# Kernel tuning notes

Measured on AMD Instinct MI355X. Metric: run time of the kernel, lower is better.

## Reference

```python
import jax, jax.numpy as jnp
import numpy as np

N = 50000
E = 800000
IN_DIM, HID, HEADS, OUT_DIM = 32, 64, 4, 128
HC = HID * HEADS  # 256
LN_EPS = 1e-5
NEG_SLOPE = 0.2


def setup_inputs() -> dict:
    key = jax.random.key(0)
    ks = jax.random.split(key, 16)
    s = 0.05
    inp = {
        "x": jax.random.normal(ks[0], (N, IN_DIM), dtype=jnp.float32),
        "edge_index": jax.random.randint(ks[1], (2, E), 0, N, dtype=jnp.int32),
        # input projection
        "W_in": jax.random.normal(ks[2], (IN_DIM, HID), dtype=jnp.float32) * s,
        "b_in": jnp.zeros((HID,), dtype=jnp.float32),
        # GAT layer 0: in=HID, out=HID per head, HEADS heads
        "lin0_w": jax.random.normal(ks[3], (HID, HC), dtype=jnp.float32) * s,
        "att0_src": jax.random.normal(ks[4], (HEADS, HID), dtype=jnp.float32) * s,
        "att0_dst": jax.random.normal(ks[5], (HEADS, HID), dtype=jnp.float32) * s,
        "bias0": jnp.zeros((HC,), dtype=jnp.float32),
        # GAT layer 1: in=HC, out=HID per head
        "lin1_w": jax.random.normal(ks[6], (HC, HC), dtype=jnp.float32) * s,
        "att1_src": jax.random.normal(ks[7], (HEADS, HID), dtype=jnp.float32) * s,
        "att1_dst": jax.random.normal(ks[8], (HEADS, HID), dtype=jnp.float32) * s,
        "bias1": jnp.zeros((HC,), dtype=jnp.float32),
        # output projection + layernorm
        "W_out": jax.random.normal(ks[9], (HC, OUT_DIM), dtype=jnp.float32) * s,
        "b_out": jnp.zeros((OUT_DIM,), dtype=jnp.float32),
        "ln_gamma": jnp.ones((OUT_DIM,), dtype=jnp.float32),
        "ln_beta": jnp.zeros((OUT_DIM,), dtype=jnp.float32),
    }
    return inp


def _gat_conv(x, src, dst, lin_w, att_src, att_dst, bias):
    # x: [N, F_in]; src/dst: [E'] (self-loops included)
    h = (x @ lin_w).reshape(N, HEADS, HID)           # [N, H, C]
    a_src = jnp.einsum("nhc,hc->nh", h, att_src)      # [N, H]
    a_dst = jnp.einsum("nhc,hc->nh", h, att_dst)      # [N, H]
    e = a_src[src] + a_dst[dst]                        # [E', H]
    e = jnp.where(e > 0, e, NEG_SLOPE * e)             # leaky_relu(0.2)
    # segment softmax over incoming edges per destination
    m = jax.ops.segment_max(e, dst, num_segments=N)    # [N, H]
    p = jnp.exp(e - m[dst])
    denom = jax.ops.segment_sum(p, dst, num_segments=N)
    alpha = p / (denom[dst] + 1e-16)                   # [E', H]
    msg = h[src] * alpha[:, :, None]                   # [E', H, C]
    out = jax.ops.segment_sum(msg, dst, num_segments=N)  # [N, H, C]
    return out.reshape(N, HC) + bias


def reference(x, edge_index, W_in, b_in, lin0_w, att0_src, att0_dst, bias0,
              lin1_w, att1_src, att1_dst, bias1, W_out, b_out, ln_gamma, ln_beta):
    # add self-loops (PyG GATConv default)
    loops = jnp.arange(N, dtype=edge_index.dtype)
    src = jnp.concatenate([edge_index[0], loops])
    dst = jnp.concatenate([edge_index[1], loops])

    h = jax.nn.elu(x @ W_in + b_in)
    h = jax.nn.elu(_gat_conv(h, src, dst, lin0_w, att0_src, att0_dst, bias0))
    h = jax.nn.elu(_gat_conv(h, src, dst, lin1_w, att1_src, att1_dst, bias1))
    h = h @ W_out + b_out
    mu = jnp.mean(h, axis=-1, keepdims=True)
    var = jnp.mean((h - mu) ** 2, axis=-1, keepdims=True)
    return (h - mu) * jax.lax.rsqrt(var + LN_EPS) * ln_gamma + ln_beta
```

## Files before the change

### kernel.cpp

```cpp
#include <hip/hip_runtime.h>
#include <cstdint>

#define N_NODES 50000
#define N_EDGES 800000
#define EP (N_EDGES + N_NODES)
#define IN_DIM 32
#define HID 64
#define HEADS 4
#define HC 256
#define OUT_DIM 128
#define NEG_SLOPE 0.2f
#define LN_EPS 1e-5f
#define SCAN_B 1024
#define NB ((N_NODES + SCAN_B - 1) / SCAN_B)

typedef __attribute__((ext_vector_type(8))) short bf16x8;
typedef __attribute__((ext_vector_type(16))) float f32x16;

__device__ __forceinline__ unsigned bf16rne(float f) {
    unsigned u = __float_as_uint(f);
    return (u + 0x7fffu + ((u >> 16) & 1u)) >> 16;
}
__device__ __forceinline__ unsigned pack_bf2(float a, float b) {
    return bf16rne(a) | (bf16rne(b) << 16);
}
__device__ __forceinline__ float bf_lo(unsigned w) { return __uint_as_float(w << 16); }
__device__ __forceinline__ float bf_hi(unsigned w) { return __uint_as_float(w & 0xffff0000u); }

__global__ void k_in_proj(const float* __restrict__ x, const float* __restrict__ W,
                          const float* __restrict__ b, unsigned short* __restrict__ out) {
    int g = blockIdx.x * blockDim.x + threadIdx.x;
    int n = g >> 6, j = g & 63;
    const float* xr = x + n * IN_DIM;
    float acc = b[j];
#pragma unroll
    for (int k = 0; k < IN_DIM; ++k) acc += xr[k] * W[k * HID + j];
    acc = acc > 0.f ? acc : (__expf(acc) - 1.f);
    out[g] = (unsigned short)bf16rne(acc);
}

__global__ void k_wpack(const float* __restrict__ w0, const float* __restrict__ w1,
                        const float* __restrict__ w2, unsigned short* __restrict__ p0,
                        unsigned short* __restrict__ p1, unsigned short* __restrict__ p2) {
    int g = blockIdx.x * blockDim.x + threadIdx.x;
    if (g < HID * HC) {
        int k = g >> 8, n = g & 255;
        p0[(((k >> 3) * HC) + n) * 8 + (k & 7)] = (unsigned short)bf16rne(w0[g]);
    } else if (g < HID * HC + HC * HC) {
        int t = g - HID * HC;
        int k = t >> 8, n = t & 255;
        p1[(((k >> 3) * HC) + n) * 8 + (k & 7)] = (unsigned short)bf16rne(w1[t]);
    } else if (g < HID * HC + HC * HC + HC * OUT_DIM) {
        int t = g - HID * HC - HC * HC;
        int k = t >> 7, n = t & 127;
        p2[(((k >> 3) * OUT_DIM) + n) * 8 + (k & 7)] = (unsigned short)bf16rne(w2[t]);
    }
}

template <int K>
__global__ __launch_bounds__(256) void k_gemm_lin(
        const unsigned short* __restrict__ A, const unsigned short* __restrict__ Bp,
        unsigned short* __restrict__ hh) {
    const int lane = threadIdx.x & 63;
    const int quad = lane >> 5, c = lane & 31;
    const int wave = threadIdx.x >> 6;
    const int m0 = blockIdx.x * 64 + (wave >> 1) * 32;
    const int cb = (wave & 1) * 128;
    f32x16 acc[4];
#pragma unroll
    for (int nt = 0; nt < 4; ++nt)
#pragma unroll
        for (int i = 0; i < 16; ++i) acc[nt][i] = 0.f;
    int mrow = m0 + c; if (mrow >= N_NODES) mrow = N_NODES - 1;
    const size_t abase = (size_t)mrow * K + quad * 8;
    for (int k0 = 0; k0 < K; k0 += 16) {
        bf16x8 af = *(const bf16x8*)(A + abase + k0);
        const unsigned short* bk = Bp + ((size_t)(k0 >> 3) + quad) * (HC * 8);
#pragma unroll
        for (int nt = 0; nt < 4; ++nt) {
            bf16x8 bf = *(const bf16x8*)(bk + (cb + nt * 32 + c) * 8);
            acc[nt] = __builtin_amdgcn_mfma_f32_32x32x16_bf16(af, bf, acc[nt], 0, 0, 0);
        }
    }
#pragma unroll
    for (int reg = 0; reg < 16; ++reg) {
        int row = (reg & 3) + 8 * (reg >> 2) + 4 * quad;
        int m = m0 + row;
        if (m < N_NODES) {
            size_t base = (size_t)m * HC + cb + c;
#pragma unroll
            for (int nt = 0; nt < 4; ++nt)
                hh[base + nt * 32] = (unsigned short)bf16rne(acc[nt][reg]);
        }
    }
}

__global__ void k_att_dots(const unsigned short* __restrict__ hh,
                           const float* __restrict__ att_s, const float* __restrict__ att_d,
                           float* __restrict__ a_src, float* __restrict__ a_dst) {
    int wid = (blockIdx.x * blockDim.x + threadIdx.x) >> 6;
    int lane = threadIdx.x & 63;
    int node = wid * 2 + (lane >> 5);
    int c0 = (lane & 31) * 8;
    int h = (lane & 31) >> 3;
    uint4 raw = *(const uint4*)(hh + (size_t)node * HC + c0);
    float as = 0.f, ad = 0.f;
#pragma unroll
    for (int t = 0; t < 4; ++t) {
        unsigned w = ((const unsigned*)&raw)[t];
        float v0 = __uint_as_float(w << 16);
        float v1 = __uint_as_float(w & 0xffff0000u);
        int cc = (c0 & 63) + t * 2;
        as += v0 * att_s[h * HID + cc] + v1 * att_s[h * HID + cc + 1];
        ad += v0 * att_d[h * HID + cc] + v1 * att_d[h * HID + cc + 1];
    }
#pragma unroll
    for (int m = 1; m < 8; m <<= 1) {
        as += __shfl_xor(as, m, 64);
        ad += __shfl_xor(ad, m, 64);
    }
    if ((lane & 7) == 0) {
        a_src[node * HEADS + h] = as;
        a_dst[node * HEADS + h] = ad;
    }
}

__global__ void k_hist(const int* __restrict__ ei, int* __restrict__ counts) {
    int e = blockIdx.x * blockDim.x + threadIdx.x;
    if (e >= EP) return;
    int d = (e < N_EDGES) ? ei[N_EDGES + e] : (e - N_EDGES);
    atomicAdd(&counts[d], 1);
}

__global__ void k_scan1(const int* __restrict__ counts, int* __restrict__ chunk_excl,
                        int* __restrict__ bsum) {
    __shared__ int buf[SCAN_B];
    int i = blockIdx.x * SCAN_B + threadIdx.x;
    int v = (i < N_NODES) ? counts[i] : 0;
    buf[threadIdx.x] = v;
    __syncthreads();
    for (int off = 1; off < SCAN_B; off <<= 1) {
        int t = (threadIdx.x >= off) ? buf[threadIdx.x - off] : 0;
        __syncthreads();
        buf[threadIdx.x] += t;
        __syncthreads();
    }
    if (i < N_NODES) chunk_excl[i] = buf[threadIdx.x] - v;
    if (threadIdx.x == SCAN_B - 1) bsum[blockIdx.x] = buf[SCAN_B - 1];
}

__global__ void k_scan3(const int* __restrict__ chunk_excl, const int* __restrict__ bsum,
                        int* __restrict__ row_ptr, int* __restrict__ cursor) {
    __shared__ int sbase;
    if (threadIdx.x < 64) {
        int v = (threadIdx.x < blockIdx.x) ? bsum[threadIdx.x] : 0;
#pragma unroll
        for (int mk = 1; mk < 64; mk <<= 1) v += __shfl_xor(v, mk, 64);
        if (threadIdx.x == 0) sbase = v;
    }
    __syncthreads();
    int i = blockIdx.x * SCAN_B + threadIdx.x;
    if (i < N_NODES) {
        int v = chunk_excl[i] + sbase;
        row_ptr[i] = v;
        cursor[i] = v;
    }
    if (i == 0) row_ptr[N_NODES] = EP;
}

__global__ void k_scatter(const int* __restrict__ ei, int* __restrict__ cursor,
                          int* __restrict__ esrc) {
    int e = blockIdx.x * blockDim.x + threadIdx.x;
    if (e >= EP) return;
    int s, d;
    if (e < N_EDGES) { s = ei[e]; d = ei[N_EDGES + e]; } else { s = d = e - N_EDGES; }
    int pos = atomicAdd(&cursor[d], 1);
    esrc[pos] = s;
}

__global__ __launch_bounds__(256) void k_gat_agg(
        const int* __restrict__ row_ptr, const int* __restrict__ esrc,
        const unsigned short* __restrict__ hh, const float* __restrict__ a_src,
        const float* __restrict__ a_dst, const float* __restrict__ bias,
        unsigned short* __restrict__ out) {
    const int wave = threadIdx.x >> 6;
    const int lane = threadIdx.x & 63;
    const int d = blockIdx.x * 4 + wave;
    const int h = lane >> 4;
    const int j = lane * 4;
    const float ad = a_dst[d * HEADS + h];
    const int beg = row_ptr[d], end = row_ptr[d + 1];
    float4 acc = {0.f, 0.f, 0.f, 0.f};
    float psum = 0.f;
    for (int base = beg; base < end; base += 64) {
        int cnt = end - base; if (cnt > 64) cnt = 64;
        int idx = base + lane;
        int myv = esrc[idx < end ? idx : end - 1];
        int i = 0;
        for (; i + 4 <= cnt; i += 4) {
            int s0 = __shfl(myv, i, 64);
            int s1 = __shfl(myv, i + 1, 64);
            int s2 = __shfl(myv, i + 2, 64);
            int s3 = __shfl(myv, i + 3, 64);
            float as0 = a_src[s0 * HEADS + h];
            float as1 = a_src[s1 * HEADS + h];
            float as2 = a_src[s2 * HEADS + h];
            float as3 = a_src[s3 * HEADS + h];
            uint2 g0 = *(const uint2*)(hh + (size_t)s0 * HC + j);
            uint2 g1 = *(const uint2*)(hh + (size_t)s1 * HC + j);
            uint2 g2 = *(const uint2*)(hh + (size_t)s2 * HC + j);
            uint2 g3 = *(const uint2*)(hh + (size_t)s3 * HC + j);
            float e0 = as0 + ad; e0 = e0 > 0.f ? e0 : NEG_SLOPE * e0;
            float e1 = as1 + ad; e1 = e1 > 0.f ? e1 : NEG_SLOPE * e1;
            float e2 = as2 + ad; e2 = e2 > 0.f ? e2 : NEG_SLOPE * e2;
            float e3 = as3 + ad; e3 = e3 > 0.f ? e3 : NEG_SLOPE * e3;
            float p0 = __expf(e0), p1 = __expf(e1), p2 = __expf(e2), p3 = __expf(e3);
            psum += (p0 + p1) + (p2 + p3);
            acc.x += p0 * bf_lo(g0.x) + p1 * bf_lo(g1.x) + p2 * bf_lo(g2.x) + p3 * bf_lo(g3.x);
            acc.y += p0 * bf_hi(g0.x) + p1 * bf_hi(g1.x) + p2 * bf_hi(g2.x) + p3 * bf_hi(g3.x);
            acc.z += p0 * bf_lo(g0.y) + p1 * bf_lo(g1.y) + p2 * bf_lo(g2.y) + p3 * bf_lo(g3.y);
            acc.w += p0 * bf_hi(g0.y) + p1 * bf_hi(g1.y) + p2 * bf_hi(g2.y) + p3 * bf_hi(g3.y);
        }
        for (; i < cnt; ++i) {
            int s0 = __shfl(myv, i, 64);
            float as0 = a_src[s0 * HEADS + h];
            uint2 g0 = *(const uint2*)(hh + (size_t)s0 * HC + j);
            float e0 = as0 + ad; e0 = e0 > 0.f ? e0 : NEG_SLOPE * e0;
            float p0 = __expf(e0);
            psum += p0;
            acc.x += p0 * bf_lo(g0.x);
            acc.y += p0 * bf_hi(g0.x);
            acc.z += p0 * bf_lo(g0.y);
            acc.w += p0 * bf_hi(g0.y);
        }
    }
    const float inv = 1.f / (psum + 1e-16f);
    const float4 bb = *(const float4*)(bias + j);
    float4 v;
    v.x = acc.x * inv + bb.x; v.y = acc.y * inv + bb.y;
    v.z = acc.z * inv + bb.z; v.w = acc.w * inv + bb.w;
    v.x = v.x > 0.f ? v.x : (__expf(v.x) - 1.f);
    v.y = v.y > 0.f ? v.y : (__expf(v.y) - 1.f);
    v.z = v.z > 0.f ? v.z : (__expf(v.z) - 1.f);
    v.w = v.w > 0.f ? v.w : (__expf(v.w) - 1.f);
    uint2 pk;
    pk.x = pack_bf2(v.x, v.y);
    pk.y = pack_bf2(v.z, v.w);
    *(uint2*)(out + (size_t)d * HC + j) = pk;
}

__global__ __launch_bounds__(256) void k_gemm_out(
        const unsigned short* __restrict__ A, const unsigned short* __restrict__ Bp,
        const float* __restrict__ b, const float* __restrict__ gamma,
        const float* __restrict__ beta, float* __restrict__ out) {
    const int lane = threadIdx.x & 63;
    const int quad = lane >> 5, c = lane & 31;
    const int m0 = blockIdx.x * 128 + (threadIdx.x >> 6) * 32;
    f32x16 acc[4];
#pragma unroll
    for (int nt = 0; nt < 4; ++nt)
#pragma unroll
        for (int i = 0; i < 16; ++i) acc[nt][i] = 0.f;
    int mrow = m0 + c; if (mrow >= N_NODES) mrow = N_NODES - 1;
    const size_t abase = (size_t)mrow * HC + quad * 8;
    for (int k0 = 0; k0 < HC; k0 += 16) {
        bf16x8 af = *(const bf16x8*)(A + abase + k0);
        const unsigned short* bk = Bp + ((size_t)(k0 >> 3) + quad) * (OUT_DIM * 8);
#pragma unroll
        for (int nt = 0; nt < 4; ++nt) {
            bf16x8 bf = *(const bf16x8*)(bk + (nt * 32 + c) * 8);
            acc[nt] = __builtin_amdgcn_mfma_f32_32x32x16_bf16(af, bf, acc[nt], 0, 0, 0);
        }
    }
    float bb[4], gg[4], be[4];
#pragma unroll
    for (int nt = 0; nt < 4; ++nt) {
        int col = nt * 32 + c;
        bb[nt] = b[col]; gg[nt] = gamma[col]; be[nt] = beta[col];
    }
#pragma unroll
    for (int reg = 0; reg < 16; ++reg) {
        int row = (reg & 3) + 8 * (reg >> 2) + 4 * quad;
        int m = m0 + row;
        float v[4];
        float s = 0.f, s2 = 0.f;
#pragma unroll
        for (int nt = 0; nt < 4; ++nt) {
            v[nt] = acc[nt][reg] + bb[nt];
            s += v[nt]; s2 += v[nt] * v[nt];
        }
#pragma unroll
        for (int mk = 1; mk < 32; mk <<= 1) {
            s += __shfl_xor(s, mk, 64);
            s2 += __shfl_xor(s2, mk, 64);
        }
        float mu = s * (1.f / OUT_DIM);
        float var = s2 * (1.f / OUT_DIM) - mu * mu;
        float inv = rsqrtf(var + LN_EPS);
        if (m < N_NODES) {
            size_t base = (size_t)m * OUT_DIM + c;
#pragma unroll
            for (int nt = 0; nt < 4; ++nt)
                out[base + nt * 32] = (v[nt] - mu) * inv * gg[nt] + be[nt];
        }
    }
}

extern "C" void kernel_launch(void* const* d_in, const int* in_sizes, int n_in,
                              void* d_out, int out_size, void* d_ws, size_t ws_size,
                              hipStream_t stream) {
    const float* x        = (const float*)d_in[0];
    const int*   ei       = (const int*)  d_in[1];
    const float* W_in     = (const float*)d_in[2];
    const float* b_in     = (const float*)d_in[3];
    const float* lin0_w   = (const float*)d_in[4];
    const float* att0_src = (const float*)d_in[5];
    const float* att0_dst = (const float*)d_in[6];
    const float* bias0    = (const float*)d_in[7];
    const float* lin1_w   = (const float*)d_in[8];
    const float* att1_src = (const float*)d_in[9];
    const float* att1_dst = (const float*)d_in[10];
    const float* bias1    = (const float*)d_in[11];
    const float* W_out    = (const float*)d_in[12];
    const float* b_out    = (const float*)d_in[13];
    const float* ln_gamma = (const float*)d_in[14];
    const float* ln_beta  = (const float*)d_in[15];
    float* out = (float*)d_out;

    unsigned short* us = (unsigned short*)d_ws;
    unsigned short* h_in_bf = us;
    unsigned short* hh_bf   = h_in_bf + (size_t)N_NODES * HID;
    unsigned short* feat_bf = hh_bf + (size_t)N_NODES * HC;
    unsigned short* p0      = feat_bf + (size_t)N_NODES * HC;
    unsigned short* p1      = p0 + HID * HC;
    unsigned short* p2      = p1 + HC * HC;
    float* a_src = (float*)(p2 + HC * OUT_DIM);
    float* a_dst = a_src + (size_t)N_NODES * HEADS;
    int* counts     = (int*)(a_dst + (size_t)N_NODES * HEADS);
    int* chunk_excl = counts + N_NODES;
    int* bsum       = chunk_excl + N_NODES;
    int* row_ptr    = bsum + NB;
    int* cursor     = row_ptr + N_NODES + 1;
    int* esrc       = cursor + N_NODES;

    k_in_proj<<<(N_NODES * HID) / 256, 256, 0, stream>>>(x, W_in, b_in, h_in_bf);
    k_wpack<<<(HID * HC + HC * HC + HC * OUT_DIM + 255) / 256, 256, 0, stream>>>(
        lin0_w, lin1_w, W_out, p0, p1, p2);

    hipMemsetAsync(counts, 0, N_NODES * sizeof(int), stream);
    k_hist<<<(EP + 255) / 256, 256, 0, stream>>>(ei, counts);
    k_scan1<<<NB, SCAN_B, 0, stream>>>(counts, chunk_excl, bsum);
    k_scan3<<<NB, SCAN_B, 0, stream>>>(chunk_excl, bsum, row_ptr, cursor);
    k_scatter<<<(EP + 255) / 256, 256, 0, stream>>>(ei, cursor, esrc);

    const int lin_grid = (N_NODES + 63) / 64;
    const int out_grid = (N_NODES + 127) / 128;
    const int dots_grid = N_NODES / 8;

    k_gemm_lin<HID><<<lin_grid, 256, 0, stream>>>(h_in_bf, p0, hh_bf);
    k_att_dots<<<dots_grid, 256, 0, stream>>>(hh_bf, att0_src, att0_dst, a_src, a_dst);
    k_gat_agg<<<N_NODES / 4, 256, 0, stream>>>(row_ptr, esrc, hh_bf, a_src, a_dst,
                                               bias0, feat_bf);

    k_gemm_lin<HC><<<lin_grid, 256, 0, stream>>>(feat_bf, p1, hh_bf);
    k_att_dots<<<dots_grid, 256, 0, stream>>>(hh_bf, att1_src, att1_dst, a_src, a_dst);
    k_gat_agg<<<N_NODES / 4, 256, 0, stream>>>(row_ptr, esrc, hh_bf, a_src, a_dst,
                                               bias1, feat_bf);

    k_gemm_out<<<out_grid, 256, 0, stream>>>(feat_bf, p2, b_out, ln_gamma, ln_beta, out);
}
```

Baseline: 411.8 us.

## Fold attention dots into GEMM, drop scatter atomics, unroll aggregation by eight

Precomputes W·att_src and W·att_dst as an extra packed bf16 B tile, so the linear GEMM also emits a_src/a_dst through one more MFMA per k-step on odd waves. That removes the separate attention-dot kernels and their re-read of hh. The histogram now records each edge's rank from its atomicAdd, so the scatter writes to row_ptr+rank without a second atomic pass. The aggregation loop is unrolled to 8 edges with unsigned index maths and an fmax-based leaky relu, at the cost of bf16 rounding of the attention weights and an extra EP-sized rank buffer.

Measured after the change: 377.3 us. 1.09x faster.

```diff
diff --git a/kernel.cpp b/kernel.cpp
--- a/kernel.cpp
+++ b/kernel.cpp
@@ -57,10 +57,24 @@
     }
 }
 
+__global__ void k_att_w(const float* __restrict__ w, const float* __restrict__ as,
+                        const float* __restrict__ ad, unsigned short* __restrict__ ext,
+                        int K) {
+    int t = blockIdx.x * blockDim.x + threadIdx.x;
+    if (t >= K * 8) return;
+    int k = t >> 3, col = t & 7, h = col & 3;
+    const float* att = (col < 4) ? as : ad;
+    float acc = 0.f;
+#pragma unroll 4
+    for (int c = 0; c < HID; ++c) acc += w[k * HC + h * HID + c] * att[h * HID + c];
+    ext[(k >> 3) * 256 + col * 8 + (k & 7)] = (unsigned short)bf16rne(acc);
+}
+
 template <int K>
 __global__ __launch_bounds__(256) void k_gemm_lin(
         const unsigned short* __restrict__ A, const unsigned short* __restrict__ Bp,
-        unsigned short* __restrict__ hh) {
+        const unsigned short* __restrict__ Ext, unsigned short* __restrict__ hh,
+        float* __restrict__ a_src, float* __restrict__ a_dst) {
     const int lane = threadIdx.x & 63;
     const int quad = lane >> 5, c = lane & 31;
     const int wave = threadIdx.x >> 6;
@@ -71,6 +85,9 @@
     for (int nt = 0; nt < 4; ++nt)
 #pragma unroll
         for (int i = 0; i < 16; ++i) acc[nt][i] = 0.f;
+    f32x16 acce;
+#pragma unroll
+    for (int i = 0; i < 16; ++i) acce[i] = 0.f;
     int mrow = m0 + c; if (mrow >= N_NODES) mrow = N_NODES - 1;
     const size_t abase = (size_t)mrow * K + quad * 8;
     for (int k0 = 0; k0 < K; k0 += 16) {
@@ -81,6 +98,10 @@
             bf16x8 bf = *(const bf16x8*)(bk + (cb + nt * 32 + c) * 8);
             acc[nt] = __builtin_amdgcn_mfma_f32_32x32x16_bf16(af, bf, acc[nt], 0, 0, 0);
         }
+        if (wave & 1) {
+            bf16x8 bfe = *(const bf16x8*)(Ext + ((k0 >> 3) + quad) * 256 + c * 8);
+            acce = __builtin_amdgcn_mfma_f32_32x32x16_bf16(af, bfe, acce, 0, 0, 0);
+        }
     }
 #pragma unroll
     for (int reg = 0; reg < 16; ++reg) {
@@ -91,45 +112,21 @@
 #pragma unroll
             for (int nt = 0; nt < 4; ++nt)
                 hh[base + nt * 32] = (unsigned short)bf16rne(acc[nt][reg]);
-        }
-    }
-}
-
-__global__ void k_att_dots(const unsigned short* __restrict__ hh,
-                           const float* __restrict__ att_s, const float* __restrict__ att_d,
-                           float* __restrict__ a_src, float* __restrict__ a_dst) {
-    int wid = (blockIdx.x * blockDim.x + threadIdx.x) >> 6;
-    int lane = threadIdx.x & 63;
-    int node = wid * 2 + (lane >> 5);
-    int c0 = (lane & 31) * 8;
-    int h = (lane & 31) >> 3;
-    uint4 raw = *(const uint4*)(hh + (size_t)node * HC + c0);
-    float as = 0.f, ad = 0.f;
-#pragma unroll
-    for (int t = 0; t < 4; ++t) {
-        unsigned w = ((const unsigned*)&raw)[t];
-        float v0 = __uint_as_float(w << 16);
-        float v1 = __uint_as_float(w & 0xffff0000u);
-        int cc = (c0 & 63) + t * 2;
-        as += v0 * att_s[h * HID + cc] + v1 * att_s[h * HID + cc + 1];
-        ad += v0 * att_d[h * HID + cc] + v1 * att_d[h * HID + cc + 1];
-    }
-#pragma unroll
-    for (int m = 1; m < 8; m <<= 1) {
-        as += __shfl_xor(as, m, 64);
-        ad += __shfl_xor(ad, m, 64);
-    }
-    if ((lane & 7) == 0) {
-        a_src[node * HEADS + h] = as;
-        a_dst[node * HEADS + h] = ad;
-    }
-}
-
-__global__ void k_hist(const int* __restrict__ ei, int* __restrict__ counts) {
+            if ((wave & 1) && c < 8) {
+                float v = acce[reg];
+                if (c < 4) a_src[m * HEADS + c] = v;
+                else       a_dst[m * HEADS + (c - 4)] = v;
+            }
+        }
+    }
+}
+
+__global__ void k_hist(const int* __restrict__ ei, int* __restrict__ counts,
+                       int* __restrict__ rank) {
     int e = blockIdx.x * blockDim.x + threadIdx.x;
     if (e >= EP) return;
     int d = (e < N_EDGES) ? ei[N_EDGES + e] : (e - N_EDGES);
-    atomicAdd(&counts[d], 1);
+    rank[e] = atomicAdd(&counts[d], 1);
 }
 
 __global__ void k_scan1(const int* __restrict__ counts, int* __restrict__ chunk_excl,
@@ -150,7 +147,7 @@
 }
 
 __global__ void k_scan3(const int* __restrict__ chunk_excl, const int* __restrict__ bsum,
-                        int* __restrict__ row_ptr, int* __restrict__ cursor) {
+                        int* __restrict__ row_ptr) {
     __shared__ int sbase;
     if (threadIdx.x < 64) {
         int v = (threadIdx.x < blockIdx.x) ? bsum[threadIdx.x] : 0;
@@ -160,22 +157,17 @@
     }
     __syncthreads();
     int i = blockIdx.x * SCAN_B + threadIdx.x;
-    if (i < N_NODES) {
-        int v = chunk_excl[i] + sbase;
-        row_ptr[i] = v;
-        cursor[i] = v;
-    }
+    if (i < N_NODES) row_ptr[i] = chunk_excl[i] + sbase;
     if (i == 0) row_ptr[N_NODES] = EP;
 }
 
-__global__ void k_scatter(const int* __restrict__ ei, int* __restrict__ cursor,
-                          int* __restrict__ esrc) {
+__global__ void k_scatter(const int* __restrict__ ei, const int* __restrict__ row_ptr,
+                          const int* __restrict__ rank, int* __restrict__ esrc) {
     int e = blockIdx.x * blockDim.x + threadIdx.x;
     if (e >= EP) return;
     int s, d;
     if (e < N_EDGES) { s = ei[e]; d = ei[N_EDGES + e]; } else { s = d = e - N_EDGES; }
-    int pos = atomicAdd(&cursor[d], 1);
-    esrc[pos] = s;
+    esrc[row_ptr[d] + rank[e]] = s;
 }
 
 __global__ __launch_bounds__(256) void k_gat_agg(
@@ -187,8 +179,8 @@
     const int lane = threadIdx.x & 63;
     const int d = blockIdx.x * 4 + wave;
     const int h = lane >> 4;
-    const int j = lane * 4;
-    const float ad = a_dst[d * HEADS + h];
+    const unsigned j = (unsigned)(lane * 4);
+    const float ad = a_dst[((unsigned)d << 2) + h];
     const int beg = row_ptr[d], end = row_ptr[d + 1];
     float4 acc = {0.f, 0.f, 0.f, 0.f};
     float psum = 0.f;
@@ -197,35 +189,47 @@
         int idx = base + lane;
         int myv = esrc[idx < end ? idx : end - 1];
         int i = 0;
-        for (; i + 4 <= cnt; i += 4) {
-            int s0 = __shfl(myv, i, 64);
-            int s1 = __shfl(myv, i + 1, 64);
-            int s2 = __shfl(myv, i + 2, 64);
-            int s3 = __shfl(myv, i + 3, 64);
-            float as0 = a_src[s0 * HEADS + h];
-            float as1 = a_src[s1 * HEADS + h];
-            float as2 = a_src[s2 * HEADS + h];
-            float as3 = a_src[s3 * HEADS + h];
-            uint2 g0 = *(const uint2*)(hh + (size_t)s0 * HC + j);
-            uint2 g1 = *(const uint2*)(hh + (size_t)s1 * HC + j);
-            uint2 g2 = *(const uint2*)(hh + (size_t)s2 * HC + j);
-            uint2 g3 = *(const uint2*)(hh + (size_t)s3 * HC + j);
-            float e0 = as0 + ad; e0 = e0 > 0.f ? e0 : NEG_SLOPE * e0;
-            float e1 = as1 + ad; e1 = e1 > 0.f ? e1 : NEG_SLOPE * e1;
-            float e2 = as2 + ad; e2 = e2 > 0.f ? e2 : NEG_SLOPE * e2;
-            float e3 = as3 + ad; e3 = e3 > 0.f ? e3 : NEG_SLOPE * e3;
+        for (; i + 8 <= cnt; i += 8) {
+            int s0 = __shfl(myv, i, 64),     s1 = __shfl(myv, i + 1, 64);
+            int s2 = __shfl(myv, i + 2, 64), s3 = __shfl(myv, i + 3, 64);
+            int s4 = __shfl(myv, i + 4, 64), s5 = __shfl(myv, i + 5, 64);
+            int s6 = __shfl(myv, i + 6, 64), s7 = __shfl(myv, i + 7, 64);
+            float as0 = a_src[((unsigned)s0 << 2) + h], as1 = a_src[((unsigned)s1 << 2) + h];
+            float as2 = a_src[((unsigned)s2 << 2) + h], as3 = a_src[((unsigned)s3 << 2) + h];
+            float as4 = a_src[((unsigned)s4 << 2) + h], as5 = a_src[((unsigned)s5 << 2) + h];
+            float as6 = a_src[((unsigned)s6 << 2) + h], as7 = a_src[((unsigned)s7 << 2) + h];
+            uint2 g0 = *(const uint2*)(hh + (((unsigned)s0 << 8) + j));
+            uint2 g1 = *(const uint2*)(hh + (((unsigned)s1 << 8) + j));
+            uint2 g2 = *(const uint2*)(hh + (((unsigned)s2 << 8) + j));
+            uint2 g3 = *(const uint2*)(hh + (((unsigned)s3 << 8) + j));
+            uint2 g4 = *(const uint2*)(hh + (((unsigned)s4 << 8) + j));
+            uint2 g5 = *(const uint2*)(hh + (((unsigned)s5 << 8) + j));
+            uint2 g6 = *(const uint2*)(hh + (((unsigned)s6 << 8) + j));
+            uint2 g7 = *(const uint2*)(hh + (((unsigned)s7 << 8) + j));
+            float e0 = as0 + ad, e1 = as1 + ad, e2 = as2 + ad, e3 = as3 + ad;
+            float e4 = as4 + ad, e5 = as5 + ad, e6 = as6 + ad, e7 = as7 + ad;
+            e0 = fmaxf(e0, NEG_SLOPE * e0); e1 = fmaxf(e1, NEG_SLOPE * e1);
+            e2 = fmaxf(e2, NEG_SLOPE * e2); e3 = fmaxf(e3, NEG_SLOPE * e3);
+            e4 = fmaxf(e4, NEG_SLOPE * e4); e5 = fmaxf(e5, NEG_SLOPE * e5);
+            e6 = fmaxf(e6, NEG_SLOPE * e6); e7 = fmaxf(e7, NEG_SLOPE * e7);
             float p0 = __expf(e0), p1 = __expf(e1), p2 = __expf(e2), p3 = __expf(e3);
-            psum += (p0 + p1) + (p2 + p3);
-            acc.x += p0 * bf_lo(g0.x) + p1 * bf_lo(g1.x) + p2 * bf_lo(g2.x) + p3 * bf_lo(g3.x);
-            acc.y += p0 * bf_hi(g0.x) + p1 * bf_hi(g1.x) + p2 * bf_hi(g2.x) + p3 * bf_hi(g3.x);
-            acc.z += p0 * bf_lo(g0.y) + p1 * bf_lo(g1.y) + p2 * bf_lo(g2.y) + p3 * bf_lo(g3.y);
-            acc.w += p0 * bf_hi(g0.y) + p1 * bf_hi(g1.y) + p2 * bf_hi(g2.y) + p3 * bf_hi(g3.y);
+            float p4 = __expf(e4), p5 = __expf(e5), p6 = __expf(e6), p7 = __expf(e7);
+            psum += ((p0 + p1) + (p2 + p3)) + ((p4 + p5) + (p6 + p7));
+            acc.x += p0 * bf_lo(g0.x) + p1 * bf_lo(g1.x) + p2 * bf_lo(g2.x) + p3 * bf_lo(g3.x)
+                   + p4 * bf_lo(g4.x) + p5 * bf_lo(g5.x) + p6 * bf_lo(g6.x) + p7 * bf_lo(g7.x);
+            acc.y += p0 * bf_hi(g0.x) + p1 * bf_hi(g1.x) + p2 * bf_hi(g2.x) + p3 * bf_hi(g3.x)
+                   + p4 * bf_hi(g4.x) + p5 * bf_hi(g5.x) + p6 * bf_hi(g6.x) + p7 * bf_hi(g7.x);
+            acc.z += p0 * bf_lo(g0.y) + p1 * bf_lo(g1.y) + p2 * bf_lo(g2.y) + p3 * bf_lo(g3.y)
+                   + p4 * bf_lo(g4.y) + p5 * bf_lo(g5.y) + p6 * bf_lo(g6.y) + p7 * bf_lo(g7.y);
+            acc.w += p0 * bf_hi(g0.y) + p1 * bf_hi(g1.y) + p2 * bf_hi(g2.y) + p3 * bf_hi(g3.y)
+                   + p4 * bf_hi(g4.y) + p5 * bf_hi(g5.y) + p6 * bf_hi(g6.y) + p7 * bf_hi(g7.y);
         }
         for (; i < cnt; ++i) {
             int s0 = __shfl(myv, i, 64);
-            float as0 = a_src[s0 * HEADS + h];
-            uint2 g0 = *(const uint2*)(hh + (size_t)s0 * HC + j);
-            float e0 = as0 + ad; e0 = e0 > 0.f ? e0 : NEG_SLOPE * e0;
+            float as0 = a_src[((unsigned)s0 << 2) + h];
+            uint2 g0 = *(const uint2*)(hh + (((unsigned)s0 << 8) + j));
+            float e0 = as0 + ad;
+            e0 = fmaxf(e0, NEG_SLOPE * e0);
             float p0 = __expf(e0);
             psum += p0;
             acc.x += p0 * bf_lo(g0.x);
@@ -334,36 +338,38 @@
     unsigned short* p0      = feat_bf + (size_t)N_NODES * HC;
     unsigned short* p1      = p0 + HID * HC;
     unsigned short* p2      = p1 + HC * HC;
-    float* a_src = (float*)(p2 + HC * OUT_DIM);
+    unsigned short* ext0    = p2 + HC * OUT_DIM;
+    unsigned short* ext1    = ext0 + 2048;
+    float* a_src = (float*)(ext1 + 8192);
     float* a_dst = a_src + (size_t)N_NODES * HEADS;
     int* counts     = (int*)(a_dst + (size_t)N_NODES * HEADS);
     int* chunk_excl = counts + N_NODES;
     int* bsum       = chunk_excl + N_NODES;
     int* row_ptr    = bsum + NB;
-    int* cursor     = row_ptr + N_NODES + 1;
-    int* esrc       = cursor + N_NODES;
+    int* rank       = row_ptr + N_NODES + 1;
+    int* esrc       = rank + EP;
 
     k_in_proj<<<(N_NODES * HID) / 256, 256, 0, stream>>>(x, W_in, b_in, h_in_bf);
     k_wpack<<<(HID * HC + HC * HC + HC * OUT_DIM + 255) / 256, 256, 0, stream>>>(
         lin0_w, lin1_w, W_out, p0, p1, p2);
+    hipMemsetAsync(ext0, 0, (2048 + 8192) * sizeof(unsigned short), stream);
+    k_att_w<<<(HID * 8 + 255) / 256, 256, 0, stream>>>(lin0_w, att0_src, att0_dst, ext0, HID);
+    k_att_w<<<(HC * 8 + 255) / 256, 256, 0, stream>>>(lin1_w, att1_src, att1_dst, ext1, HC);
 
     hipMemsetAsync(counts, 0, N_NODES * sizeof(int), stream);
-    k_hist<<<(EP + 255) / 256, 256, 0, stream>>>(ei, counts);
+    k_hist<<<(EP + 255) / 256, 256, 0, stream>>>(ei, counts, rank);
     k_scan1<<<NB, SCAN_B, 0, stream>>>(counts, chunk_excl, bsum);
-    k_scan3<<<NB, SCAN_B, 0, stream>>>(chunk_excl, bsum, row_ptr, cursor);
-    k_scatter<<<(EP + 255) / 256, 256, 0, stream>>>(ei, cursor, esrc);
+    k_scan3<<<NB, SCAN_B, 0, stream>>>(chunk_excl, bsum, row_ptr);
+    k_scatter<<<(EP + 255) / 256, 256, 0, stream>>>(ei, row_ptr, rank, esrc);
 
     const int lin_grid = (N_NODES + 63) / 64;
     const int out_grid = (N_NODES + 127) / 128;
-    const int dots_grid = N_NODES / 8;
-
-    k_gemm_lin<HID><<<lin_grid, 256, 0, stream>>>(h_in_bf, p0, hh_bf);
-    k_att_dots<<<dots_grid, 256, 0, stream>>>(hh_bf, att0_src, att0_dst, a_src, a_dst);
+
+    k_gemm_lin<HID><<<lin_grid, 256, 0, stream>>>(h_in_bf, p0, ext0, hh_bf, a_src, a_dst);
     k_gat_agg<<<N_NODES / 4, 256, 0, stream>>>(row_ptr, esrc, hh_bf, a_src, a_dst,
                                                bias0, feat_bf);
 
-    k_gemm_lin<HC><<<lin_grid, 256, 0, stream>>>(feat_bf, p1, hh_bf);
-    k_att_dots<<<dots_grid, 256, 0, stream>>>(hh_bf, att1_src, att1_dst, a_src, a_dst);
+    k_gemm_lin<HC><<<lin_grid, 256, 0, stream>>>(feat_bf, p1, ext1, hh_bf, a_src, a_dst);
     k_gat_agg<<<N_NODES / 4, 256, 0, stream>>>(row_ptr, esrc, hh_bf, a_src, a_dst,
                                                bias1, feat_bf);
 
```
